# Performance work log

Hardware: AMD Instinct MI355X
Metric: run time of the kernel (lower is better)

## Reference

```python
import jax, jax.numpy as jnp
import numpy as np

B, V, L, D, H, W = 4, 2, 8192, 768, 12, 512  # batch, views, seq, d_model, heads, window


def _layernorm(x, g, b, eps=1e-5):
    # matches torch LayerNorm computed in fp32 then cast back
    x32 = x.astype(jnp.float32)
    m = x32.mean(-1, keepdims=True)
    v = ((x32 - m) ** 2).mean(-1, keepdims=True)
    return ((x32 - m) * jax.lax.rsqrt(v + eps) * g + b).astype(x.dtype)


def _mha(q_in, k_in, v_in, wqkv, bqkv, wo, bo, h):
    # torch nn.MultiheadAttention (eval mode, no mask). inputs [..., S, d]
    d = q_in.shape[-1]
    hd = d // h
    scale = 1.0 / np.sqrt(hd)
    q = (q_in @ wqkv[:d].T + bqkv[:d]).reshape(*q_in.shape[:-1], h, hd)
    k = (k_in @ wqkv[d:2 * d].T + bqkv[d:2 * d]).reshape(*k_in.shape[:-1], h, hd)
    v = (v_in @ wqkv[2 * d:].T + bqkv[2 * d:]).reshape(*v_in.shape[:-1], h, hd)
    scores = jnp.einsum('...qhd,...khd->...hqk', q, k) * scale
    a = jax.nn.softmax(scores, axis=-1)
    o = jnp.einsum('...hqk,...khd->...qhd', a, v).reshape(q_in.shape)
    return o @ wo.T + bo


def reference(x, ln1_g, ln1_b, ln2_g, ln2_b,
              a1_wqkv, a1_bqkv, a1_wo, a1_bo,
              a2_wqkv, a2_bqkv, a2_wo, a2_bo,
              fc_w, fc_b, proj_w, proj_b, index):
    b, v, l, c = x.shape
    y = _layernorm(x, ln1_g, ln1_b)
    shifted = (index % 2 == 1)  # index is a static Python int
    xs = jnp.roll(x, W // 2, axis=2) if shifted else x
    p = l // W
    xw = xs.reshape(b, v, p, W, c)  # window partition (only x is rolled, as in source)
    yw = y.reshape(b, v, p, W, c)
    # cross-view windowed attention: Q=norm view i, K=norm view j, V=raw view i
    v1 = _mha(yw[:, 0], yw[:, 1], xw[:, 0], a1_wqkv, a1_bqkv, a1_wo, a1_bo, H)
    v2 = _mha(yw[:, 1], yw[:, 0], xw[:, 1], a2_wqkv, a2_bqkv, a2_wo, a2_bo, H)
    att = jnp.stack([v1, v2], axis=1).reshape(b, v, l, c)
    if shifted:
        att = jnp.roll(att, -(W // 2), axis=2)
    x = x + att
    y2 = _layernorm(x, ln2_g, ln2_b)
    h = y2 @ fc_w.T + fc_b
    h = h * jax.nn.sigmoid(1.702 * h)  # fast GELU
    return x + (h @ proj_w.T + proj_b)


def setup_inputs() -> dict:
    key = jax.random.key(0)
    ks = jax.random.split(key, 10)
    s = 0.02
    return {
        'x': jax.random.normal(ks[0], (B, V, L, D), jnp.float32),
        'ln1_g': jnp.ones((D,), jnp.float32),
        'ln1_b': jnp.zeros((D,), jnp.float32),
        'ln2_g': jnp.ones((D,), jnp.float32),
        'ln2_b': jnp.zeros((D,), jnp.float32),
        'a1_wqkv': jax.random.normal(ks[1], (3 * D, D), jnp.float32) * s,
        'a1_bqkv': jnp.zeros((3 * D,), jnp.float32),
        'a1_wo': jax.random.normal(ks[2], (D, D), jnp.float32) * s,
        'a1_bo': jnp.zeros((D,), jnp.float32),
        'a2_wqkv': jax.random.normal(ks[3], (3 * D, D), jnp.float32) * s,
        'a2_bqkv': jnp.zeros((3 * D,), jnp.float32),
        'a2_wo': jax.random.normal(ks[4], (D, D), jnp.float32) * s,
        'a2_bo': jnp.zeros((D,), jnp.float32),
        'fc_w': jax.random.normal(ks[5], (4 * D, D), jnp.float32) * s,
        'fc_b': jnp.zeros((4 * D,), jnp.float32),
        'proj_w': jax.random.normal(ks[6], (D, 4 * D), jnp.float32) * s,
        'proj_b': jnp.zeros((D,), jnp.float32),
        'index': 0,
    }
```

## Files before the change

kernel.cpp:

```cpp
#include <hip/hip_runtime.h>
#include <hip/hip_bf16.h>

typedef __bf16 bf16x8 __attribute__((ext_vector_type(8)));
typedef float  f32x4  __attribute__((ext_vector_type(4)));
typedef short  s16x4  __attribute__((ext_vector_type(4)));
typedef unsigned short u16;

#define L2E 1.44269504088896f
#define SBAR  __builtin_amdgcn_s_barrier()
#define SCHED __builtin_amdgcn_sched_barrier(0)

static __device__ __forceinline__ u16 f2bf(float f) {
  unsigned u = __builtin_bit_cast(unsigned, f);
  u += 0x7fffu + ((u >> 16) & 1u);
  return (u16)(u >> 16);
}

static __device__ __forceinline__ void gld_lds16(const void* g, void* l) {
  __builtin_amdgcn_global_load_lds((const __attribute__((address_space(1))) unsigned*)g,
                                   (__attribute__((address_space(3))) unsigned*)l, 16, 0, 0);
}

__global__ __launch_bounds__(256)
void cvtk(const float* __restrict__ s, u16* __restrict__ d, int n) {
  const int i = (blockIdx.x * 256 + threadIdx.x) * 4;
  if (i >= n) return;
  const float4 f = *(const float4*)(s + i);
  s16x4 p;
  p[0] = (short)f2bf(f.x); p[1] = (short)f2bf(f.y);
  p[2] = (short)f2bf(f.z); p[3] = (short)f2bf(f.w);
  *(s16x4*)(d + i) = p;
}

__global__ __launch_bounds__(256)
void lnk(const float* __restrict__ x, const float* __restrict__ gw,
         const float* __restrict__ bw, u16* __restrict__ y,
         u16* __restrict__ xv, int viewmajor) {
  const int lane = threadIdx.x & 63;
  const int tok = blockIdx.x * 4 + (threadIdx.x >> 6);
  const float* xr = x + (size_t)tok * 768;
  float4 v[3];
  float s = 0.f, sq = 0.f;
#pragma unroll
  for (int j = 0; j < 3; ++j) {
    v[j] = *(const float4*)(xr + j * 256 + lane * 4);
    s  += v[j].x + v[j].y + v[j].z + v[j].w;
    sq += v[j].x * v[j].x + v[j].y * v[j].y + v[j].z * v[j].z + v[j].w * v[j].w;
  }
#pragma unroll
  for (int o = 1; o < 64; o <<= 1) { s += __shfl_xor(s, o); sq += __shfl_xor(sq, o); }
  const float mean = s * (1.f / 768.f);
  const float var  = sq * (1.f / 768.f) - mean * mean;
  const float rstd = rsqrtf(var + 1e-5f);
  size_t yrow = (size_t)tok;
  if (viewmajor) {
    const int b_ = tok >> 14, vv = (tok >> 13) & 1, l_ = tok & 8191;
    yrow = ((size_t)((vv << 2) + b_) << 13) + l_;
  }
#pragma unroll
  for (int j = 0; j < 3; ++j) {
    const float4 g4 = *(const float4*)(gw + j * 256 + lane * 4);
    const float4 b4 = *(const float4*)(bw + j * 256 + lane * 4);
    s16x4 py;
    py[0] = (short)f2bf((v[j].x - mean) * rstd * g4.x + b4.x);
    py[1] = (short)f2bf((v[j].y - mean) * rstd * g4.y + b4.y);
    py[2] = (short)f2bf((v[j].z - mean) * rstd * g4.z + b4.z);
    py[3] = (short)f2bf((v[j].w - mean) * rstd * g4.w + b4.w);
    *(s16x4*)(y + yrow * 768 + j * 256 + lane * 4) = py;
    if (xv) {
      s16x4 px;
      px[0] = (short)f2bf(v[j].x); px[1] = (short)f2bf(v[j].y);
      px[2] = (short)f2bf(v[j].z); px[3] = (short)f2bf(v[j].w);
      *(s16x4*)(xv + yrow * 768 + j * 256 + lane * 4) = px;
    }
  }
}

template<int MODE>
__global__ __launch_bounds__(512, 2)
void gemm_bt(const u16* __restrict__ A,
             const u16* __restrict__ B1, const u16* __restrict__ B2,
             const float* __restrict__ b1, const float* __restrict__ b2,
             void* __restrict__ C1, void* __restrict__ C2,
             int N, int K,
             const float* __restrict__ xres, const int* __restrict__ idxp) {
  __shared__ char lds[131072];
  const int t = threadIdx.x;
  const int lane = t & 63;
  const int wid = t >> 6;
  const int wm = wid >> 2, wn = wid & 3;

  const int cpx = gridDim.x >> 3;
  const int bid = (blockIdx.x & 7) * cpx + (blockIdx.x >> 3);
  const int Ntiles = N >> 8;
  const int PPB = Ntiles << 3;
  const int panel = bid / PPB;
  const int rem = bid - panel * PPB;
  const int nt = rem >> 3;
  const int mt = (panel << 3) + (rem & 7);

  const u16* Bsel = B1; const float* bias = b1; int ntl = nt;
  if constexpr (MODE == 5) {
    if (nt >= 3) { Bsel = B2; bias = b2; ntl = nt - 3; }
  } else if constexpr (MODE == 6 || MODE == 7) {
    if (mt >= 128) { Bsel = B2; bias = b2; }
  }

  const int urow = t >> 3;
  const int koff = ((t & 7) ^ (urow & 7)) << 3;
  const u16* Asrc = A + (size_t)(mt * 256 + urow) * K + koff;
  const u16* Bsrc = Bsel + (size_t)(ntl * 256 + urow) * K + koff;
  const int wdst = wid << 10;

  auto stgA = [&](int d, int kt, int u0) {
    char* base = (char*)lds + d * 32768 + wdst;
    gld_lds16(Asrc + (size_t)(u0 * 64) * K + kt * 64, base + u0 * 8192);
    gld_lds16(Asrc + (size_t)(u0 * 64 + 64) * K + kt * 64, base + u0 * 8192 + 8192);
  };
  auto stgB = [&](int d, int kt, int u0) {
    char* base = (char*)lds + 65536 + d * 32768 + wdst;
    gld_lds16(Bsrc + (size_t)(u0 * 64) * K + kt * 64, base + u0 * 8192);
    gld_lds16(Bsrc + (size_t)(u0 * 64 + 64) * K + kt * 64, base + u0 * 8192 + 8192);
  };

  const int c15 = lane & 15, g = lane >> 4;
  const int axor = c15 & 7;
  const char* LAb = (char*)lds + (wm * 128 + c15) * 128;
  const char* LBb = (char*)lds + 65536 + (wn * 64 + c15) * 128;
  bf16x8 av[4][2], bv[4][2];
  auto rdA = [&](int d, int mh) {
#pragma unroll
    for (int m = 0; m < 4; ++m)
#pragma unroll
      for (int ks = 0; ks < 2; ++ks)
        av[m][ks] = *(const bf16x8*)(LAb + d * 32768 + (mh * 64 + m * 16) * 128 +
                                     (((ks << 2) | g) ^ axor) * 16);
  };
  auto rdB = [&](int d) {
#pragma unroll
    for (int n = 0; n < 4; ++n)
#pragma unroll
      for (int ks = 0; ks < 2; ++ks)
        bv[n][ks] = *(const bf16x8*)(LBb + d * 32768 + (n * 16) * 128 +
                                     (((ks << 2) | g) ^ axor) * 16);
  };

  f32x4 acc[8][4] = {};
  auto QD = [&](int mh, int nh) {
    __builtin_amdgcn_s_setprio(1);
#pragma unroll
    for (int ks = 0; ks < 2; ++ks)
#pragma unroll
      for (int m = 0; m < 4; ++m)
#pragma unroll
        for (int n = 0; n < 2; ++n)
          acc[mh * 4 + m][nh * 2 + n] = __builtin_amdgcn_mfma_f32_16x16x32_bf16(
              av[m][ks], bv[nh * 2 + n][ks], acc[mh * 4 + m][nh * 2 + n], 0, 0, 0);
    __builtin_amdgcn_s_setprio(0);
  };

  const int nk = K >> 6, niter = nk >> 1, last = nk - 1;

  stgA(0, 0, 0); stgA(0, 0, 2); stgB(0, 0, 0); stgB(0, 0, 2);
  stgB(1, 1, 0); stgB(1, 1, 2); stgA(1, 1, 0);
  asm volatile("s_waitcnt vmcnt(6)" ::: "memory");
  SBAR;

  for (int it = 0; it < niter; ++it) {
    const int i2 = it * 2;
    const int t1 = (i2 + 1 < nk) ? i2 + 1 : last;
    const int t2 = (i2 + 2 < nk) ? i2 + 2 : last;
    const int t3 = (i2 + 3 < nk) ? i2 + 3 : last;

    rdA(0, 0); rdB(0); stgA(1, t1, 2);
    SCHED; SBAR;
    QD(0, 0);
    stgB(0, t2, 0);
    SCHED; SBAR;
    QD(0, 1);
    rdA(0, 1); stgB(0, t2, 2);
    SCHED; SBAR;
    QD(1, 1);
    stgA(0, t2, 0);
    asm volatile("s_waitcnt vmcnt(6)" ::: "memory");
    SCHED; SBAR;
    QD(1, 0);
    rdA(1, 0); rdB(1); stgA(0, t2, 2);
    SCHED; SBAR;
    QD(0, 0);
    stgB(1, t3, 0);
    SCHED; SBAR;
    QD(0, 1);
    rdA(1, 1); stgB(1, t3, 2);
    SCHED; SBAR;
    QD(1, 1);
    stgA(1, t3, 0);
    asm volatile("s_waitcnt vmcnt(6)" ::: "memory");
    SCHED; SBAR;
    QD(1, 0);
  }

  int shift = 0;
  if constexpr (MODE == 7) shift = (idxp[0] & 1) ? 256 : 0;

  const int rb0 = mt * 256 + wm * 128 + (g << 2);
  const int cb_nt = (MODE == 5) ? ntl : nt;
  const int cbase = cb_nt * 256 + wn * 64 + c15;
#pragma unroll
  for (int mi = 0; mi < 8; ++mi) {
    const int row = rb0 + mi * 16;
#pragma unroll
    for (int nj = 0; nj < 4; ++nj) {
      const int col = cbase + nj * 16;
      const float bvv = bias[col];
      if constexpr (MODE == 3) {
        u16* C = (u16*)C1;
#pragma unroll
        for (int r = 0; r < 4; ++r) {
          const float u = acc[mi][nj][r] + bvv;
          const float e = __builtin_amdgcn_exp2f(-2.45546693f * u);
          C[(size_t)(row + r) * N + col] = f2bf(u / (1.f + e));
        }
      } else if constexpr (MODE == 4) {
        float* C = (float*)C1;
#pragma unroll
        for (int r = 0; r < 4; ++r) {
          const size_t idx = (size_t)(row + r) * 768 + col;
          C[idx] = C[idx] + acc[mi][nj][r] + bvv;
        }
      } else if constexpr (MODE == 5) {
        u16* C = (u16*)(nt >= 3 ? C2 : C1);
#pragma unroll
        for (int r = 0; r < 4; ++r)
          C[(size_t)(row + r) * 768 + col] = f2bf(acc[mi][nj][r] + bvv);
      } else if constexpr (MODE == 6) {
        u16* C = (u16*)(row >= 32768 ? C2 : C1);
        const int r32 = row & 32767;
        const int hh = col >> 6, dd = col & 63;
        const int b_ = r32 >> 13, l_ = r32 & 8191;
        s16x4 pk;
#pragma unroll
        for (int r = 0; r < 4; ++r) pk[r] = (short)f2bf(acc[mi][nj][r] + bvv);
        *(s16x4*)(C + (((size_t)((b_ * 12 + hh) << 6) + dd) << 13) + l_) = pk;
      } else {
        float* C = (float*)C1;
        const int att = row >> 15;
        const int r32 = row & 32767;
        const int b_ = r32 >> 13, p_ = r32 & 8191;
        const int l0 = (p_ - shift) & 8191;
        const size_t rbase = ((size_t)((b_ << 1) + att) << 13) + l0;
#pragma unroll
        for (int r = 0; r < 4; ++r) {
          const size_t idx = (rbase + r) * 768 + col;
          C[idx] = xres[idx] + acc[mi][nj][r] + bvv;
        }
      }
    }
  }
}

__global__ __launch_bounds__(512, 2)
void attnk(const u16* __restrict__ Q1, const u16* __restrict__ K1, const u16* __restrict__ V1,
           const u16* __restrict__ Q2, const u16* __restrict__ K2, const u16* __restrict__ V2,
           u16* __restrict__ O, const int* __restrict__ idxp) {
  __shared__ char lds[131072];
  const int t = threadIdx.x;
  const int lane = t & 63;
  const int c = lane & 15, g = lane >> 4;
  const int wid = t >> 6;
  int bb = blockIdx.x;
  const int h = bb % 12; bb /= 12;
  const int w = bb & 15; bb >>= 4;
  const int b = bb & 3;
  const int a = bb >> 2;
  const int shift = (idxp[0] & 1) ? 256 : 0;

  const u16* Q  = a ? Q2 : Q1;
  const u16* Kb = a ? K2 : K1;
  const u16* Vt = a ? V2 : V1;
  const int kbase = b * 8192 + w * 512;
  const u16* Vts = Vt + ((size_t)(b * 12 + h) << 19);

  const int qrow0 = b * 8192 + w * 512 + wid * 64;
  bf16x8 qf[4][2];
#pragma unroll
  for (int q = 0; q < 4; ++q)
#pragma unroll
    for (int hf = 0; hf < 2; ++hf)
      qf[q][hf] = *(const bf16x8*)(Q + (size_t)(qrow0 + q * 16 + c) * 768 + h * 64 + hf * 32 + g * 8);

  {
    const int r0 = t >> 3, ch = t & 7;
    char* kdst = (char*)lds + (wid << 10);
#pragma unroll
    for (int p = 0; p < 8; ++p) {
      const int row = p * 64 + r0;
      gld_lds16(Kb + (size_t)(kbase + row) * 768 + h * 64 + ((ch ^ (row & 7)) << 3),
                kdst + p * 8192);
    }
    char* vdst = (char*)lds + 65536 + (wid << 10);
#pragma unroll
    for (int p = 0; p < 8; ++p) {
      const int vrow = p * 8 + wid;
      const int cg = lane ^ (vrow & 7);
      const int l = (w * 512 + cg * 8 - shift) & 8191;
      gld_lds16(Vts + (size_t)vrow * 8192 + l, vdst + p * 8192);
    }
  }
  __syncthreads();

  f32x4 oacc[4][4] = {};
  f32x4 psum[4] = {};
  const float CEXP = 0.125f * L2E;
  const char* LK = (char*)lds;
  const char* LV = (char*)lds + 65536;

  for (int kt = 0; kt < 32; ++kt) {
    const int krow = kt * 16 + c;
    const int ksw = krow & 7;
    const bf16x8 kf0 = *(const bf16x8*)(LK + krow * 128 + ((g ^ ksw) << 4));
    const bf16x8 kf1 = *(const bf16x8*)(LK + krow * 128 + (((4 | g) ^ ksw) << 4));
    s16x4 vf[4];
#pragma unroll
    for (int df = 0; df < 4; ++df) {
      const int vr = df * 16 + c;
      vf[df] = *(const s16x4*)(LV + vr * 1024 +
                               (((kt * 2 + (g >> 1)) ^ (vr & 7)) << 4) + ((g & 1) << 3));
    }

    const f32x4 z = {0.f, 0.f, 0.f, 0.f};
    s16x4 pk[4];
#pragma unroll
    for (int q = 0; q < 4; ++q) {
      f32x4 sc2 = __builtin_amdgcn_mfma_f32_16x16x32_bf16(kf0, qf[q][0], z, 0, 0, 0);
      sc2 = __builtin_amdgcn_mfma_f32_16x16x32_bf16(kf1, qf[q][1], sc2, 0, 0, 0);
      f32x4 pv;
      pv[0] = __builtin_amdgcn_exp2f(sc2[0] * CEXP);
      pv[1] = __builtin_amdgcn_exp2f(sc2[1] * CEXP);
      pv[2] = __builtin_amdgcn_exp2f(sc2[2] * CEXP);
      pv[3] = __builtin_amdgcn_exp2f(sc2[3] * CEXP);
      psum[q] += pv;
      pk[q][0] = (short)f2bf(pv[0]);
      pk[q][1] = (short)f2bf(pv[1]);
      pk[q][2] = (short)f2bf(pv[2]);
      pk[q][3] = (short)f2bf(pv[3]);
    }
#pragma unroll
    for (int df = 0; df < 4; ++df)
#pragma unroll
      for (int q = 0; q < 4; ++q)
        oacc[df][q] = __builtin_amdgcn_mfma_f32_16x16x16bf16_1k(vf[df], pk[q], oacc[df][q], 0, 0, 0);
  }

  const size_t orow0 = (size_t)(a * 32768 + qrow0);
#pragma unroll
  for (int q = 0; q < 4; ++q) {
    float ss = psum[q][0] + psum[q][1] + psum[q][2] + psum[q][3];
    ss += __shfl_xor(ss, 16);
    ss += __shfl_xor(ss, 32);
    const float inv = 1.f / ss;
#pragma unroll
    for (int df = 0; df < 4; ++df) {
      s16x4 po;
#pragma unroll
      for (int r = 0; r < 4; ++r) po[r] = (short)f2bf(oacc[df][q][r] * inv);
      *(s16x4*)(O + (orow0 + q * 16 + c) * 768 + h * 64 + df * 16 + g * 4) = po;
    }
  }
}

extern "C" void kernel_launch(void* const* d_in, const int* in_sizes, int n_in,
                              void* d_out, int out_size, void* d_ws, size_t ws_size,
                              hipStream_t stream) {
  const float* x       = (const float*)d_in[0];
  const float* ln1_g   = (const float*)d_in[1];
  const float* ln1_b   = (const float*)d_in[2];
  const float* ln2_g   = (const float*)d_in[3];
  const float* ln2_b   = (const float*)d_in[4];
  const float* a1_wqkv = (const float*)d_in[5];
  const float* a1_bqkv = (const float*)d_in[6];
  const float* a1_wo   = (const float*)d_in[7];
  const float* a1_bo   = (const float*)d_in[8];
  const float* a2_wqkv = (const float*)d_in[9];
  const float* a2_bqkv = (const float*)d_in[10];
  const float* a2_wo   = (const float*)d_in[11];
  const float* a2_bo   = (const float*)d_in[12];
  const float* fc_w    = (const float*)d_in[13];
  const float* fc_b    = (const float*)d_in[14];
  const float* proj_w  = (const float*)d_in[15];
  const float* proj_b  = (const float*)d_in[16];
  const int*   idxp    = (const int*)d_in[17];
  float* out = (float*)d_out;

  u16* p = (u16*)d_ws;
  u16* w1  = p; p += (size_t)2304 * 768;
  u16* w2  = p; p += (size_t)2304 * 768;
  u16* wo1 = p; p += (size_t)768 * 768;
  u16* wo2 = p; p += (size_t)768 * 768;
  u16* fcw = p; p += (size_t)3072 * 768;
  u16* pjw = p; p += (size_t)768 * 3072;
  u16* y   = p; p += (size_t)65536 * 768;
  u16* xv  = p; p += (size_t)65536 * 768;
  u16* Q1  = p; p += (size_t)32768 * 768;
  u16* K1  = p; p += (size_t)32768 * 768;
  u16* V1  = p; p += (size_t)32768 * 768;
  u16* Q2  = p; p += (size_t)32768 * 768;
  u16* K2  = p; p += (size_t)32768 * 768;
  u16* V2  = p; p += (size_t)32768 * 768;
  u16* Ob  = p; p += (size_t)65536 * 768;
  u16* hb  = Q1;

  cvtk<<<1728, 256, 0, stream>>>(a1_wqkv, w1, 2304 * 768);
  cvtk<<<1728, 256, 0, stream>>>(a2_wqkv, w2, 2304 * 768);
  cvtk<<<576,  256, 0, stream>>>(a1_wo, wo1, 768 * 768);
  cvtk<<<576,  256, 0, stream>>>(a2_wo, wo2, 768 * 768);
  cvtk<<<2304, 256, 0, stream>>>(fc_w, fcw, 3072 * 768);
  cvtk<<<2304, 256, 0, stream>>>(proj_w, pjw, 768 * 3072);

  lnk<<<16384, 256, 0, stream>>>(x, ln1_g, ln1_b, y, xv, 1);

  const size_t VS = (size_t)32768 * 768;

  gemm_bt<5><<<768, 512, 0, stream>>>(y, w1, w2 + 768 * 768,
                                      a1_bqkv, a2_bqkv + 768,
                                      Q1, K2, 1536, 768, nullptr, idxp);
  gemm_bt<5><<<768, 512, 0, stream>>>(y + VS, w1 + 768 * 768, w2,
                                      a1_bqkv + 768, a2_bqkv,
                                      K1, Q2, 1536, 768, nullptr, idxp);
  gemm_bt<6><<<768, 512, 0, stream>>>(xv, w1 + 2 * 768 * 768, w2 + 2 * 768 * 768,
                                      a1_bqkv + 1536, a2_bqkv + 1536,
                                      V1, V2, 768, 768, nullptr, idxp);

  attnk<<<1536, 512, 0, stream>>>(Q1, K1, V1, Q2, K2, V2, Ob, idxp);

  gemm_bt<7><<<768, 512, 0, stream>>>(Ob, wo1, wo2, a1_bo, a2_bo,
                                      out, nullptr, 768, 768, x, idxp);

  lnk<<<16384, 256, 0, stream>>>(out, ln2_g, ln2_b, y, nullptr, 0);

  gemm_bt<3><<<3072, 512, 0, stream>>>(y, fcw, nullptr, fc_b, nullptr,
                                       hb, nullptr, 3072, 768, nullptr, idxp);

  gemm_bt<4><<<768, 512, 0, stream>>>(hb, pjw, nullptr, proj_b, nullptr,
                                      out, nullptr, 768, 3072, nullptr, idxp);
}
```

Measured before the change: 1.372 ms.

## Restructure GEMM main loop to four barrier phases with finer-grained staging

Splits the global-to-LDS staging helpers into single-quarter loads and reorganizes the double-buffered GEMM k-loop from eight barrier-separated phases into four. Each phase now issues two MFMA quadrants and four staged loads, with adjusted vmcnt waits. The goal is to cut barrier count and sync overhead while keeping loads overlapped with compute. The risk is that the reordered waits leave less latency hiding, or create a hazard if a buffer quarter is overwritten before all waves have read it.

```diff
diff --git a/kernel.cpp b/kernel.cpp
--- a/kernel.cpp
+++ b/kernel.cpp
@@ -112,15 +112,13 @@
   const u16* Bsrc = Bsel + (size_t)(ntl * 256 + urow) * K + koff;
   const int wdst = wid << 10;
 
-  auto stgA = [&](int d, int kt, int u0) {
-    char* base = (char*)lds + d * 32768 + wdst;
-    gld_lds16(Asrc + (size_t)(u0 * 64) * K + kt * 64, base + u0 * 8192);
-    gld_lds16(Asrc + (size_t)(u0 * 64 + 64) * K + kt * 64, base + u0 * 8192 + 8192);
+  auto stg1A = [&](int d, int kt, int q) {
+    gld_lds16(Asrc + (size_t)(q * 64) * K + kt * 64,
+              (char*)lds + d * 32768 + q * 8192 + wdst);
   };
-  auto stgB = [&](int d, int kt, int u0) {
-    char* base = (char*)lds + 65536 + d * 32768 + wdst;
-    gld_lds16(Bsrc + (size_t)(u0 * 64) * K + kt * 64, base + u0 * 8192);
-    gld_lds16(Bsrc + (size_t)(u0 * 64 + 64) * K + kt * 64, base + u0 * 8192 + 8192);
+  auto stg1B = [&](int d, int kt, int q) {
+    gld_lds16(Bsrc + (size_t)(q * 64) * K + kt * 64,
+              (char*)lds + 65536 + d * 32768 + q * 8192 + wdst);
   };
 
   const int c15 = lane & 15, g = lane >> 4;
@@ -161,43 +159,38 @@
 
   const int nk = K >> 6, niter = nk >> 1, last = nk - 1;
 
-  stgA(0, 0, 0); stgA(0, 0, 2); stgB(0, 0, 0); stgB(0, 0, 2);
-  stgB(1, 1, 0); stgB(1, 1, 2); stgA(1, 1, 0);
-  asm volatile("s_waitcnt vmcnt(6)" ::: "memory");
+  stg1A(0, 0, 0); stg1A(0, 0, 1); stg1A(0, 0, 2); stg1A(0, 0, 3);
+  stg1B(0, 0, 0); stg1B(0, 0, 1); stg1B(0, 0, 2); stg1B(0, 0, 3);
+  stg1A(1, 1, 0); stg1A(1, 1, 2); stg1B(1, 1, 0); stg1B(1, 1, 1);
+  asm volatile("s_waitcnt vmcnt(4)" ::: "memory");
   SBAR;
 
   for (int it = 0; it < niter; ++it) {
     const int i2 = it * 2;
-    const int t1 = (i2 + 1 < nk) ? i2 + 1 : last;
+    const int t1 = i2 + 1;
     const int t2 = (i2 + 2 < nk) ? i2 + 2 : last;
     const int t3 = (i2 + 3 < nk) ? i2 + 3 : last;
 
-    rdA(0, 0); rdB(0); stgA(1, t1, 2);
+    rdA(0, 0); rdB(0);
+    stg1A(1, t1, 1); stg1A(1, t1, 3); stg1B(1, t1, 2); stg1B(1, t1, 3);
+    asm volatile("s_waitcnt vmcnt(8)" ::: "memory");
     SCHED; SBAR;
-    QD(0, 0);
-    stgB(0, t2, 0);
+    QD(0, 0); QD(0, 1);
+    rdA(0, 1);
+    stg1A(0, t2, 0); stg1A(0, t2, 2); stg1B(0, t2, 0); stg1B(0, t2, 1);
+    asm volatile("s_waitcnt vmcnt(4)" ::: "memory");
     SCHED; SBAR;
-    QD(0, 1);
-    rdA(0, 1); stgB(0, t2, 2);
+    QD(1, 1); QD(1, 0);
+    rdA(1, 0); rdB(1);
+    stg1A(0, t2, 1); stg1A(0, t2, 3); stg1B(0, t2, 2); stg1B(0, t2, 3);
+    asm volatile("s_waitcnt vmcnt(8)" ::: "memory");
     SCHED; SBAR;
-    QD(1, 1);
-    stgA(0, t2, 0);
-    asm volatile("s_waitcnt vmcnt(6)" ::: "memory");
+    QD(0, 0); QD(0, 1);
+    rdA(1, 1);
+    stg1A(1, t3, 0); stg1A(1, t3, 2); stg1B(1, t3, 0); stg1B(1, t3, 1);
+    asm volatile("s_waitcnt vmcnt(4)" ::: "memory");
     SCHED; SBAR;
-    QD(1, 0);
-    rdA(1, 0); rdB(1); stgA(0, t2, 2);
-    SCHED; SBAR;
-    QD(0, 0);
-    stgB(1, t3, 0);
-    SCHED; SBAR;
-    QD(0, 1);
-    rdA(1, 1); stgB(1, t3, 2);
-    SCHED; SBAR;
-    QD(1, 1);
-    stgA(1, t3, 0);
-    asm volatile("s_waitcnt vmcnt(6)" ::: "memory");
-    SCHED; SBAR;
-    QD(1, 0);
+    QD(1, 1); QD(1, 0);
   }
 
   int shift = 0;
```

Measured after the change: 1.383 ms. About the same (+0.8%).
